# Optimization experiments

Measured on AMD Instinct MI355X. Metric: run time of the kernel, lower is better.

The kernel has to match this reference:

```python
import jax, jax.numpy as jnp
from jax import lax
import numpy as np

N_CENTER, N_NEAR, COUT = 1024, 32, 256


def fps(xyz, m):
    # farthest point sampling -> [B, m] int32 indices
    B, N, _ = xyz.shape
    dist0 = jnp.full((B, N), 1e10, xyz.dtype)
    far0 = jnp.zeros((B,), jnp.int32)

    def step(carry, _):
        dists, far = carry
        cen = jax.vmap(lambda p, i: p[i])(xyz, far)            # [B,3]
        d = jnp.sum((xyz - cen[:, None, :]) ** 2, axis=-1)     # [B,N]
        dists = jnp.minimum(dists, d)
        nxt = jnp.argmax(dists, axis=-1).astype(jnp.int32)
        return (dists, nxt), far

    _, idx = lax.scan(step, (dist0, far0), None, length=m)
    return jnp.transpose(idx)                                   # [B,m]


def knn(xyz, k):
    # euclidean kNN over all points -> [B,N,k] (stand-in for surface_knn)
    sq = jnp.sum(xyz ** 2, axis=-1)                             # [B,N]
    d = sq[:, :, None] + sq[:, None, :] - 2.0 * jnp.einsum('bnd,bmd->bnm', xyz, xyz)
    _, idx = lax.top_k(-d, k)
    return idx


def gather(x, idx):
    # index_points: x [B,N,...], idx [B,S] or [B,S,K]
    return jax.vmap(lambda p, i: p[i])(x, idx)


def point_attention(center_fea, group_fea, wq, wk, wv):
    # center_fea [B,S,Cin], group_fea [B,S,K,D] -> [B,S,COUT]
    q = jnp.einsum('bsc,ch->bsh', center_fea, wq)
    k = jnp.einsum('bskd,dh->bskh', group_fea, wk)
    v = jnp.einsum('bskd,dh->bskh', group_fea, wv)
    scores = jnp.einsum('bsh,bskh->bsk', q, k) / jnp.sqrt(jnp.asarray(COUT, q.dtype))
    attn = jax.nn.softmax(scores, axis=-1)
    return jnp.einsum('bsk,bskh->bsh', attn, v)


def _forward(xyz, mad, adj, pt, mad_fea, adj_fea, pt_fea, cst_fea,
             wq_mad, wk_mad, wv_mad, wq_adj, wk_adj, wv_adj,
             wq_pt, wk_pt, wv_pt, wq_cst, wk_cst, wv_cst):
    idx_all = knn(xyz, N_NEAR)                  # [B,N,K]
    fps_idx = fps(xyz, N_CENTER)                # [B,S]

    center_xyz = gather(xyz, fps_idx)
    center_mad = gather(mad, fps_idx)
    center_adj = gather(adj, fps_idx)
    center_pt = gather(pt, fps_idx)
    c_mad_fea = gather(mad_fea, fps_idx)
    c_adj_fea = gather(adj_fea, fps_idx)
    c_pt_fea = gather(pt_fea, fps_idx)
    c_cst_fea = gather(cst_fea, fps_idx)

    idx = gather(idx_all, fps_idx)              # [B,S,K]
    g_xyz = gather(xyz, idx)
    g_mad = gather(mad, idx)
    g_adj = gather(adj, idx)
    g_pt = gather(pt, idx)
    g_mad_fea = gather(mad_fea, idx)
    g_adj_fea = gather(adj_fea, idx)
    g_pt_fea = gather(pt_fea, idx)
    g_cst_fea = gather(cst_fea, idx)

    mad_rel = g_mad - center_mad[:, :, None, :]
    adj_cat = jnp.concatenate([g_adj, jnp.broadcast_to(center_adj[:, :, None, :], g_adj.shape)], axis=-1)
    pt_cat = jnp.concatenate([g_pt, jnp.broadcast_to(center_pt[:, :, None, :], g_pt.shape)], axis=-1)
    xyz_rel = g_xyz - center_xyz[:, :, None, :]

    g_mad_fea = jnp.concatenate([g_mad_fea, mad_rel], axis=-1)
    g_adj_fea = jnp.concatenate([g_adj_fea, adj_cat], axis=-1)
    g_pt_fea = jnp.concatenate([g_pt_fea, pt_cat], axis=-1)
    g_cst_fea = jnp.concatenate([g_cst_fea, xyz_rel], axis=-1)

    o_mad = point_attention(c_mad_fea, g_mad_fea, wq_mad, wk_mad, wv_mad)
    o_adj = point_attention(c_adj_fea, g_adj_fea, wq_adj, wk_adj, wv_adj)
    o_pt = point_attention(c_pt_fea, g_pt_fea, wq_pt, wk_pt, wv_pt)
    o_cst = point_attention(c_cst_fea, g_cst_fea, wq_cst, wk_cst, wv_cst)

    return (center_xyz, center_mad, center_adj, center_pt, o_mad, o_adj, o_pt, o_cst)


def setup_inputs() -> dict:
    key = jax.random.key(0)
    ks = jax.random.split(key, 24)
    B, N, C = 4, 4096, 128
    inp = {
        'xyz': jax.random.normal(ks[0], (B, N, 3), jnp.float32),
        'mad': jax.random.normal(ks[1], (B, N, 3), jnp.float32),
        'adj': jax.random.uniform(ks[2], (B, N, 2), jnp.float32),
        'pt': jax.random.uniform(ks[3], (B, N, 4), jnp.float32),
        'mad_fea': jax.random.normal(ks[4], (B, N, C), jnp.float32),
        'adj_fea': jax.random.normal(ks[5], (B, N, C), jnp.float32),
        'pt_fea': jax.random.normal(ks[6], (B, N, C), jnp.float32),
        'cst_fea': jax.random.normal(ks[7], (B, N, C), jnp.float32),
    }
    dims = {'wq_mad': C, 'wk_mad': C + 3, 'wv_mad': C + 3,
            'wq_adj': C, 'wk_adj': C + 4, 'wv_adj': C + 4,
            'wq_pt': C, 'wk_pt': C + 8, 'wv_pt': C + 8,
            'wq_cst': C, 'wk_cst': C + 3, 'wv_cst': C + 3}
    for i, (name, d) in enumerate(dims.items()):
        inp[name] = jax.random.normal(ks[8 + i], (d, COUT), jnp.float32) * 0.02
    return inp


def reference(xyz, mad, adj, pt, mad_fea, adj_fea, pt_fea, cst_fea,
              wq_mad, wk_mad, wv_mad, wq_adj, wk_adj, wv_adj,
              wq_pt, wk_pt, wv_pt, wq_cst, wk_cst, wv_cst):
    return _forward(xyz, mad, adj, pt, mad_fea, adj_fea, pt_fea, cst_fea,
                    wq_mad, wk_mad, wv_mad, wq_adj, wk_adj, wv_adj,
                    wq_pt, wk_pt, wv_pt, wq_cst, wk_cst, wv_cst)
```

## Files before the change

kernel.cpp:

```cpp
#include <hip/hip_runtime.h>

#define BATCH 4
#define NPTS  4096
#define NC    1024
#define KNN   32
#define CIN   128
#define CO    256
#define DP    136

#define OFF_CXYZ 0
#define OFF_CMAD (BATCH*NC*3)
#define OFF_CADJ (OFF_CMAD + BATCH*NC*3)
#define OFF_CPT  (OFF_CADJ + BATCH*NC*2)
#define OFF_OMAD (OFF_CPT  + BATCH*NC*4)
#define OFF_OADJ (OFF_OMAD + BATCH*NC*CO)
#define OFF_OPT  (OFF_OADJ + BATCH*NC*CO)
#define OFF_OCST (OFF_OPT  + BATCH*NC*CO)

typedef unsigned long long u64;

template<bool MAXI>
__device__ __forceinline__ u64 wave_red_u64(u64 k)
{
    const int oldv = MAXI ? 0 : -1;
#define DPP_STEP(C)                                                              \
    {                                                                            \
        unsigned plo = (unsigned)__builtin_amdgcn_update_dpp(oldv, (int)(unsigned)k,        C, 0xf, 0xf, false); \
        unsigned phi = (unsigned)__builtin_amdgcn_update_dpp(oldv, (int)(unsigned)(k>>32),  C, 0xf, 0xf, false); \
        u64 p = ((u64)phi << 32) | plo;                                          \
        if (MAXI ? (p > k) : (p < k)) k = p;                                     \
    }
    DPP_STEP(0x111) DPP_STEP(0x112) DPP_STEP(0x114)
    DPP_STEP(0x118) DPP_STEP(0x142) DPP_STEP(0x143)
#undef DPP_STEP
    return k;
}

__global__ __launch_bounds__(256) void fps_prep_kernel(
    const float* __restrict__ xyz, int* __restrict__ fps_idx,
    const float* __restrict__ wq_mad, const float* __restrict__ wk_mad, const float* __restrict__ wv_mad,
    const float* __restrict__ wq_adj, const float* __restrict__ wk_adj, const float* __restrict__ wv_adj,
    const float* __restrict__ wq_pt,  const float* __restrict__ wk_pt,  const float* __restrict__ wv_pt,
    const float* __restrict__ wq_cst, const float* __restrict__ wk_cst, const float* __restrict__ wv_cst,
    float* __restrict__ M, float* __restrict__ Wvp)
{
    __shared__ float4 s_xyz[NPTS];
    __shared__ u64    s_ck[2][4];
    const int t = threadIdx.x;

    if (blockIdx.x >= BATCH) {
        const int r    = blockIdx.x - BATCH;
        const int type = r / DP;
        const int row  = r - type * DP;
        const float* wq; const float* wk; const float* wv; int D;
        if (type == 0)      { wq=wq_mad; wk=wk_mad; wv=wv_mad; D=131; }
        else if (type == 1) { wq=wq_adj; wk=wk_adj; wv=wv_adj; D=132; }
        else if (type == 2) { wq=wq_pt;  wk=wk_pt;  wv=wv_pt;  D=136; }
        else                { wq=wq_cst; wk=wk_cst; wv=wv_cst; D=131; }

        Wvp[((size_t)type*DP + row)*CO + t] = (row < D) ? wv[(size_t)row*CO + t] : 0.f;

        if (row < CIN) {
            float* sq = (float*)s_xyz;
            sq[t] = wq[(size_t)row*CO + t];
            __syncthreads();
            if (t < DP) {
                float acc = 0.f;
                if (t < D) {
                    const float* wkr = wk + (size_t)t * CO;
                    for (int h = 0; h < CO; h += 4) {
                        float4 a = *(const float4*)&wkr[h];
                        float4 b4 = *(const float4*)&sq[h];
                        acc = fmaf(a.x,b4.x,acc); acc = fmaf(a.y,b4.y,acc);
                        acc = fmaf(a.z,b4.z,acc); acc = fmaf(a.w,b4.w,acc);
                    }
                }
                M[((size_t)type*CIN + row)*DP + t] = acc;
            }
        }
        return;
    }

    const int b = blockIdx.x;
    const float* xb = xyz + (size_t)b * NPTS * 3;

    float px[16], py[16], pz[16], dd[16];
    unsigned pv[16];
#pragma unroll
    for (int i = 0; i < 16; ++i) {
        int p = t + i * 256;
        px[i] = xb[p*3+0]; py[i] = xb[p*3+1]; pz[i] = xb[p*3+2];
        s_xyz[p] = make_float4(px[i], py[i], pz[i], 0.f);
        dd[i] = 1e10f;
        pv[i] = (unsigned)p;
    }
    __syncthreads();

    int far = 0;
    float cx = xb[0], cy = xb[1], cz = xb[2];
    for (int s = 0; s < NC; ++s) {
        if (t == 0) fps_idx[b*NC + s] = far;

        float    gm[4] = {-1.f, -1.f, -1.f, -1.f};
        unsigned gi[4] = {0u, 0u, 0u, 0u};
#pragma unroll
        for (int i = 0; i < 16; ++i) {
            float dx = __fsub_rn(px[i], cx);
            float dy = __fsub_rn(py[i], cy);
            float dz = __fsub_rn(pz[i], cz);
            float d  = __fadd_rn(__fadd_rn(__fmul_rn(dx,dx), __fmul_rn(dy,dy)), __fmul_rn(dz,dz));
            float nd = fminf(dd[i], d);
            dd[i] = nd;
            const int g = i >> 2;
            if (nd > gm[g]) gi[g] = pv[i];
            gm[g] = fmaxf(gm[g], nd);
        }
        bool c1 = gm[1] > gm[0]; float a0 = c1 ? gm[1] : gm[0]; unsigned b0 = c1 ? gi[1] : gi[0];
        bool c3 = gm[3] > gm[2]; float a1 = c3 ? gm[3] : gm[2]; unsigned b1 = c3 ? gi[3] : gi[2];
        bool cf = a1 > a0;       float am = cf ? a1 : a0;       unsigned bm = cf ? b1 : b0;
        u64 k = ((u64)__float_as_uint(am) << 32) | (u64)(unsigned)~bm;

        k = wave_red_u64<true>(k);

        const int buf = s & 1;
        if ((t & 63) == 63) s_ck[buf][t>>6] = k;
        __syncthreads();
        u64 k0 = s_ck[buf][0], k1 = s_ck[buf][1], k2 = s_ck[buf][2], k3 = s_ck[buf][3];
        float4 c0 = s_xyz[(int)~((unsigned)k0)];
        float4 c1v = s_xyz[(int)~((unsigned)k1)];
        float4 c2v = s_xyz[(int)~((unsigned)k2)];
        float4 c3v = s_xyz[(int)~((unsigned)k3)];
        bool m1 = k1 > k0; u64 ka = m1 ? k1 : k0; float4 ca = m1 ? c1v : c0;
        bool m3 = k3 > k2; u64 kb = m3 ? k3 : k2; float4 cb = m3 ? c3v : c2v;
        bool mf = kb > ka; u64 kw = mf ? kb : ka; float4 cw = mf ? cb : ca;
        far = (int)~((unsigned)kw);
        cx = cw.x; cy = cw.y; cz = cw.z;
    }
}

__global__ __launch_bounds__(256) void knn_kernel(const float* __restrict__ xyz,
                                                  const int* __restrict__ fps_idx,
                                                  int* __restrict__ nbr_idx)
{
    const int bs = blockIdx.x;
    const int b  = bs >> 10;
    const int t  = threadIdx.x;
    const float* xb = xyz + (size_t)b * NPTS * 3;
    const int ci = fps_idx[bs];
    const float cx = xb[ci*3], cy = xb[ci*3+1], cz = xb[ci*3+2];
    const float sqc = __fadd_rn(__fadd_rn(__fmul_rn(cx,cx), __fmul_rn(cy,cy)), __fmul_rn(cz,cz));

    u64 key[16];
#pragma unroll
    for (int i = 0; i < 16; ++i) {
        int p = t + i * 256;
        float x = xb[p*3], y = xb[p*3+1], z = xb[p*3+2];
        float sqm = __fadd_rn(__fadd_rn(__fmul_rn(x,x), __fmul_rn(y,y)), __fmul_rn(z,z));
        float dot = __fadd_rn(__fadd_rn(__fmul_rn(cx,x), __fmul_rn(cy,y)), __fmul_rn(cz,z));
        float dv  = __fsub_rn(__fadd_rn(sqc, sqm), __fmul_rn(2.0f, dot));
        unsigned u = __float_as_uint(dv);
        u ^= (unsigned)(((int)u >> 31)) | 0x80000000u;
        key[i] = ((u64)u << 32) | (unsigned)p;
    }
    u64 kmin = key[0];
#pragma unroll
    for (int i = 1; i < 16; ++i) if (key[i] < kmin) kmin = key[i];

    __shared__ u64 s_ck[2][4];

    for (int kk = 0; kk < KNN; ++kk) {
        u64 k = wave_red_u64<false>(kmin);
        const int buf = kk & 1;
        if ((t & 63) == 63) s_ck[buf][t>>6] = k;
        __syncthreads();
        u64 k0 = s_ck[buf][0], k1 = s_ck[buf][1], k2 = s_ck[buf][2], k3 = s_ck[buf][3];
        if (k1 < k0) k0 = k1;
        if (k3 < k2) k2 = k3;
        if (k2 < k0) k0 = k2;
        unsigned w = (unsigned)k0;
        if (t == 0) nbr_idx[bs*KNN + kk] = (int)w;
        if ((w & 255u) == (unsigned)t) {
#pragma unroll
            for (int i = 0; i < 16; ++i)
                if (w == (unsigned)(t + i*256)) key[i] = ~0ull;
            u64 m = key[0];
#pragma unroll
            for (int i = 1; i < 16; ++i) if (key[i] < m) m = key[i];
            kmin = m;
        }
    }
}

template<int TYPE>
__device__ __forceinline__ void attn_t(
    int b, int bs0, int ci,
    const float* __restrict__ fea, const float* __restrict__ aux,
    const float* __restrict__ Mt, const float* __restrict__ Wvpt,
    float* __restrict__ outp,
    float (*s_cf)[CIN], float (*s_u)[DP], float (*s_fea)[KNN][DP],
    float (*s_sc)[KNN], float (*s_wf)[DP], const int (*s_nbr4)[KNN])
{
    const int t = threadIdx.x, g = t >> 6, l = t & 63;
    const int l31 = l & 31, h32 = l >> 5;

    if (l < 32) {
        float4 v = *(const float4*)&fea[((size_t)(b*NPTS + ci))*CIN + l*4];
        *(float4*)&s_cf[g][l*4] = v;
    }
#pragma unroll
    for (int it = 0; it < 16; ++it) {
        int kk = it*2 + h32;
        int j  = s_nbr4[g][kk];
        float4 v = *(const float4*)&fea[((size_t)(b*NPTS + j))*CIN + l31*4];
        *(float4*)&s_fea[g][kk][l31*4] = v;
    }
    if (l < KNN) {
        int j = s_nbr4[g][l];
        float pad[8];
        if (TYPE == 0 || TYPE == 3) {
#pragma unroll
            for (int i = 0; i < 3; ++i)
                pad[i] = aux[(size_t)(b*NPTS + j)*3 + i] - aux[(size_t)(b*NPTS + ci)*3 + i];
            pad[3]=pad[4]=pad[5]=pad[6]=pad[7]=0.f;
        } else if (TYPE == 1) {
            pad[0] = aux[(size_t)(b*NPTS + j)*2 + 0];
            pad[1] = aux[(size_t)(b*NPTS + j)*2 + 1];
            pad[2] = aux[(size_t)(b*NPTS + ci)*2 + 0];
            pad[3] = aux[(size_t)(b*NPTS + ci)*2 + 1];
            pad[4]=pad[5]=pad[6]=pad[7]=0.f;
        } else {
#pragma unroll
            for (int i = 0; i < 4; ++i) pad[i]   = aux[(size_t)(b*NPTS + j)*4 + i];
#pragma unroll
            for (int i = 0; i < 4; ++i) pad[4+i] = aux[(size_t)(b*NPTS + ci)*4 + i];
        }
#pragma unroll
        for (int i = 0; i < 8; ++i) s_fea[g][l][CIN+i] = pad[i];
    }
    __syncthreads();

#pragma unroll
    for (int j = 0; j < 3; ++j) {
        int d = l + 64*j;
        if (d < DP) {
            float acc = 0.f;
            for (int c = 0; c < CIN; c += 4) {
                float4 cf4 = *(const float4*)&s_cf[g][c];
                acc = fmaf(cf4.x, Mt[(size_t)(c+0)*DP + d], acc);
                acc = fmaf(cf4.y, Mt[(size_t)(c+1)*DP + d], acc);
                acc = fmaf(cf4.z, Mt[(size_t)(c+2)*DP + d], acc);
                acc = fmaf(cf4.w, Mt[(size_t)(c+3)*DP + d], acc);
            }
            s_u[g][d] = acc;
        }
    }
    __syncthreads();

#pragma unroll
    for (int it = 0; it < 16; ++it) {
        int kk = it*2 + h32;
        float acc = 0.f;
        for (int c = l31; c < DP/4; c += 32) {
            float4 f4 = *(const float4*)&s_fea[g][kk][c*4];
            float4 u4 = *(const float4*)&s_u[g][c*4];
            acc = fmaf(f4.x,u4.x,acc); acc = fmaf(f4.y,u4.y,acc);
            acc = fmaf(f4.z,u4.z,acc); acc = fmaf(f4.w,u4.w,acc);
        }
#pragma unroll
        for (int off = 16; off; off >>= 1) acc += __shfl_xor(acc, off);
        if (l31 == 0) s_sc[g][kk] = acc * 0.0625f;
    }
    __syncthreads();

    if (l < KNN) {
        float sc = s_sc[g][l];
        float m = sc;
#pragma unroll
        for (int off = 16; off; off >>= 1) m = fmaxf(m, __shfl_xor(m, off));
        float e = expf(sc - m);
        float ssum = e;
#pragma unroll
        for (int off = 16; off; off >>= 1) ssum += __shfl_xor(ssum, off);
        s_sc[g][l] = e / ssum;
    }
    __syncthreads();

    if (l < DP/4) {
        const int d0 = l*4;
        float w0=0.f, w1=0.f, w2=0.f, w3=0.f;
#pragma unroll
        for (int k4 = 0; k4 < KNN; k4 += 4) {
            float4 a  = *(const float4*)&s_sc[g][k4];
            float4 f0 = *(const float4*)&s_fea[g][k4+0][d0];
            float4 f1 = *(const float4*)&s_fea[g][k4+1][d0];
            float4 f2 = *(const float4*)&s_fea[g][k4+2][d0];
            float4 f3 = *(const float4*)&s_fea[g][k4+3][d0];
            w0=fmaf(a.x,f0.x,w0); w1=fmaf(a.x,f0.y,w1); w2=fmaf(a.x,f0.z,w2); w3=fmaf(a.x,f0.w,w3);
            w0=fmaf(a.y,f1.x,w0); w1=fmaf(a.y,f1.y,w1); w2=fmaf(a.y,f1.z,w2); w3=fmaf(a.y,f1.w,w3);
            w0=fmaf(a.z,f2.x,w0); w1=fmaf(a.z,f2.y,w1); w2=fmaf(a.z,f2.z,w2); w3=fmaf(a.z,f2.w,w3);
            w0=fmaf(a.w,f3.x,w0); w1=fmaf(a.w,f3.y,w1); w2=fmaf(a.w,f3.z,w2); w3=fmaf(a.w,f3.w,w3);
        }
        s_wf[g][d0+0]=w0; s_wf[g][d0+1]=w1; s_wf[g][d0+2]=w2; s_wf[g][d0+3]=w3;
    }
    __syncthreads();

    float o0=0.f, o1=0.f, o2=0.f, o3=0.f;
    for (int d4 = 0; d4 < DP/4; ++d4) {
        float4 wf0 = *(const float4*)&s_wf[0][d4*4];
        float4 wf1 = *(const float4*)&s_wf[1][d4*4];
        float4 wf2 = *(const float4*)&s_wf[2][d4*4];
        float4 wf3 = *(const float4*)&s_wf[3][d4*4];
        float v0 = Wvpt[(size_t)(d4*4+0)*CO + t];
        float v1 = Wvpt[(size_t)(d4*4+1)*CO + t];
        float v2 = Wvpt[(size_t)(d4*4+2)*CO + t];
        float v3 = Wvpt[(size_t)(d4*4+3)*CO + t];
        o0=fmaf(wf0.x,v0,o0); o0=fmaf(wf0.y,v1,o0); o0=fmaf(wf0.z,v2,o0); o0=fmaf(wf0.w,v3,o0);
        o1=fmaf(wf1.x,v0,o1); o1=fmaf(wf1.y,v1,o1); o1=fmaf(wf1.z,v2,o1); o1=fmaf(wf1.w,v3,o1);
        o2=fmaf(wf2.x,v0,o2); o2=fmaf(wf2.y,v1,o2); o2=fmaf(wf2.z,v2,o2); o2=fmaf(wf2.w,v3,o2);
        o3=fmaf(wf3.x,v0,o3); o3=fmaf(wf3.y,v1,o3); o3=fmaf(wf3.z,v2,o3); o3=fmaf(wf3.w,v3,o3);
    }
    outp[(size_t)(bs0+0)*CO + t] = o0;
    outp[(size_t)(bs0+1)*CO + t] = o1;
    outp[(size_t)(bs0+2)*CO + t] = o2;
    outp[(size_t)(bs0+3)*CO + t] = o3;
    __syncthreads();
}

__global__ __launch_bounds__(256) void attn_kernel(
    const float* __restrict__ xyz, const float* __restrict__ mad,
    const float* __restrict__ adj, const float* __restrict__ pt,
    const float* __restrict__ mad_fea, const float* __restrict__ adj_fea,
    const float* __restrict__ pt_fea,  const float* __restrict__ cst_fea,
    const float* __restrict__ M, const float* __restrict__ Wvp,
    const int* __restrict__ fps_idx, const int* __restrict__ nbr_idx,
    float* __restrict__ out)
{
    __shared__ float s_cf[4][CIN];
    __shared__ float s_u[4][DP];
    __shared__ float s_fea[4][KNN][DP];
    __shared__ float s_sc[4][KNN];
    __shared__ float s_wf[4][DP];
    __shared__ int   s_nbr4[4][KNN];
    __shared__ int   s_ci4[4];

    const int bs0 = blockIdx.x * 4;
    const int b   = bs0 >> 10;
    const int t   = threadIdx.x;
    const int g   = t >> 6, l = t & 63;

    if (t < 4) s_ci4[t] = fps_idx[bs0 + t];
    if (t < 128) s_nbr4[t>>5][t&31] = nbr_idx[(bs0 + (t>>5))*KNN + (t&31)];
    __syncthreads();
    const int ci = s_ci4[g];

    if (l < 3)             out[OFF_CXYZ + (bs0+g)*3 + l]      = xyz[(size_t)(b*NPTS+ci)*3 + l];
    if (l >= 4 && l < 7)   out[OFF_CMAD + (bs0+g)*3 + (l-4)]  = mad[(size_t)(b*NPTS+ci)*3 + (l-4)];
    if (l >= 8 && l < 10)  out[OFF_CADJ + (bs0+g)*2 + (l-8)]  = adj[(size_t)(b*NPTS+ci)*2 + (l-8)];
    if (l >= 12 && l < 16) out[OFF_CPT  + (bs0+g)*4 + (l-12)] = pt[(size_t)(b*NPTS+ci)*4 + (l-12)];

    attn_t<0>(b, bs0, ci, mad_fea, mad, M + 0*CIN*DP, Wvp + 0*DP*CO, out + OFF_OMAD,
              s_cf, s_u, s_fea, s_sc, s_wf, s_nbr4);
    attn_t<1>(b, bs0, ci, adj_fea, adj, M + 1*CIN*DP, Wvp + 1*DP*CO, out + OFF_OADJ,
              s_cf, s_u, s_fea, s_sc, s_wf, s_nbr4);
    attn_t<2>(b, bs0, ci, pt_fea,  pt,  M + 2*CIN*DP, Wvp + 2*DP*CO, out + OFF_OPT,
              s_cf, s_u, s_fea, s_sc, s_wf, s_nbr4);
    attn_t<3>(b, bs0, ci, cst_fea, xyz, M + 3*CIN*DP, Wvp + 3*DP*CO, out + OFF_OCST,
              s_cf, s_u, s_fea, s_sc, s_wf, s_nbr4);
}

extern "C" void kernel_launch(void* const* d_in, const int* in_sizes, int n_in,
                              void* d_out, int out_size, void* d_ws, size_t ws_size,
                              hipStream_t stream)
{
    const float* xyz     = (const float*)d_in[0];
    const float* mad     = (const float*)d_in[1];
    const float* adj     = (const float*)d_in[2];
    const float* pt      = (const float*)d_in[3];
    const float* mad_fea = (const float*)d_in[4];
    const float* adj_fea = (const float*)d_in[5];
    const float* pt_fea  = (const float*)d_in[6];
    const float* cst_fea = (const float*)d_in[7];
    const float* wq_mad  = (const float*)d_in[8];
    const float* wk_mad  = (const float*)d_in[9];
    const float* wv_mad  = (const float*)d_in[10];
    const float* wq_adj  = (const float*)d_in[11];
    const float* wk_adj  = (const float*)d_in[12];
    const float* wv_adj  = (const float*)d_in[13];
    const float* wq_pt   = (const float*)d_in[14];
    const float* wk_pt   = (const float*)d_in[15];
    const float* wv_pt   = (const float*)d_in[16];
    const float* wq_cst  = (const float*)d_in[17];
    const float* wk_cst  = (const float*)d_in[18];
    const float* wv_cst  = (const float*)d_in[19];
    float* out = (float*)d_out;

    int*   fps_idx = (int*)d_ws;
    int*   nbr_idx = fps_idx + BATCH*NC;
    float* M       = (float*)(nbr_idx + BATCH*NC*KNN);
    float* Wvp     = M + 4*CIN*DP;

    fps_prep_kernel<<<BATCH + 4*DP, 256, 0, stream>>>(xyz, fps_idx,
        wq_mad, wk_mad, wv_mad, wq_adj, wk_adj, wv_adj,
        wq_pt, wk_pt, wv_pt, wq_cst, wk_cst, wv_cst, M, Wvp);
    knn_kernel<<<BATCH*NC, 256, 0, stream>>>(xyz, fps_idx, nbr_idx);
    attn_kernel<<<BATCH*NC/4, 256, 0, stream>>>(xyz, mad, adj, pt,
        mad_fea, adj_fea, pt_fea, cst_fea, M, Wvp, fps_idx, nbr_idx, out);
}
```

Measured before the change: 1.121 ms.

## Interleave two batches' farthest point sampling per block to share barriers

```diff
diff --git a/kernel.cpp b/kernel.cpp
--- a/kernel.cpp
+++ b/kernel.cpp
@@ -36,6 +36,29 @@
     return k;
 }
 
+__device__ __forceinline__ u64 fps_step(const float* px, const float* py, const float* pz,
+                                        float* dd, float cx, float cy, float cz, int t)
+{
+    float    gm[4] = {-1.f, -1.f, -1.f, -1.f};
+    unsigned gi[4] = {0u, 0u, 0u, 0u};
+#pragma unroll
+    for (int i = 0; i < 16; ++i) {
+        float dx = __fsub_rn(px[i], cx);
+        float dy = __fsub_rn(py[i], cy);
+        float dz = __fsub_rn(pz[i], cz);
+        float d  = __fadd_rn(__fadd_rn(__fmul_rn(dx,dx), __fmul_rn(dy,dy)), __fmul_rn(dz,dz));
+        float nd = fminf(dd[i], d);
+        dd[i] = nd;
+        const int g = i >> 2;
+        if (nd > gm[g]) gi[g] = (unsigned)(t + i*256);
+        gm[g] = fmaxf(gm[g], nd);
+    }
+    bool c1 = gm[1] > gm[0]; float a0 = c1 ? gm[1] : gm[0]; unsigned b0 = c1 ? gi[1] : gi[0];
+    bool c3 = gm[3] > gm[2]; float a1 = c3 ? gm[3] : gm[2]; unsigned b1 = c3 ? gi[3] : gi[2];
+    bool cf = a1 > a0;       float am = cf ? a1 : a0;       unsigned bm = cf ? b1 : b0;
+    return ((u64)__float_as_uint(am) << 32) | (u64)(unsigned)~bm;
+}
+
 __global__ __launch_bounds__(256) void fps_prep_kernel(
     const float* __restrict__ xyz, int* __restrict__ fps_idx,
     const float* __restrict__ wq_mad, const float* __restrict__ wk_mad, const float* __restrict__ wv_mad,
@@ -44,12 +67,13 @@
     const float* __restrict__ wq_cst, const float* __restrict__ wk_cst, const float* __restrict__ wv_cst,
     float* __restrict__ M, float* __restrict__ Wvp)
 {
-    __shared__ float4 s_xyz[NPTS];
-    __shared__ u64    s_ck[2][4];
+    __shared__ float2 s_xy[2][NPTS];
+    __shared__ float  s_z [2][NPTS];
+    __shared__ u64    s_ck[2][2][4];
     const int t = threadIdx.x;
 
-    if (blockIdx.x >= BATCH) {
-        const int r    = blockIdx.x - BATCH;
+    if (blockIdx.x >= 2) {
+        const int r    = blockIdx.x - 2;
         const int type = r / DP;
         const int row  = r - type * DP;
         const float* wq; const float* wk; const float* wv; int D;
@@ -61,7 +85,7 @@
         Wvp[((size_t)type*DP + row)*CO + t] = (row < D) ? wv[(size_t)row*CO + t] : 0.f;
 
         if (row < CIN) {
-            float* sq = (float*)s_xyz;
+            float* sq = (float*)s_xy;
             sq[t] = wq[(size_t)row*CO + t];
             __syncthreads();
             if (t < DP) {
@@ -81,60 +105,58 @@
         return;
     }
 
-    const int b = blockIdx.x;
-    const float* xb = xyz + (size_t)b * NPTS * 3;
-
-    float px[16], py[16], pz[16], dd[16];
-    unsigned pv[16];
+    const int b0 = blockIdx.x * 2, b1 = b0 + 1;
+    const float* xb0 = xyz + (size_t)b0 * NPTS * 3;
+    const float* xb1 = xyz + (size_t)b1 * NPTS * 3;
+
+    float px0[16], py0[16], pz0[16], dd0[16];
+    float px1[16], py1[16], pz1[16], dd1[16];
 #pragma unroll
     for (int i = 0; i < 16; ++i) {
         int p = t + i * 256;
-        px[i] = xb[p*3+0]; py[i] = xb[p*3+1]; pz[i] = xb[p*3+2];
-        s_xyz[p] = make_float4(px[i], py[i], pz[i], 0.f);
-        dd[i] = 1e10f;
-        pv[i] = (unsigned)p;
-    }
-    __syncthreads();
-
-    int far = 0;
-    float cx = xb[0], cy = xb[1], cz = xb[2];
+        px0[i] = xb0[p*3+0]; py0[i] = xb0[p*3+1]; pz0[i] = xb0[p*3+2];
+        px1[i] = xb1[p*3+0]; py1[i] = xb1[p*3+1]; pz1[i] = xb1[p*3+2];
+        s_xy[0][p] = make_float2(px0[i], py0[i]); s_z[0][p] = pz0[i];
+        s_xy[1][p] = make_float2(px1[i], py1[i]); s_z[1][p] = pz1[i];
+        dd0[i] = 1e10f; dd1[i] = 1e10f;
+    }
+    __syncthreads();
+
+    int farA = 0, farB = 0;
+    float cxA = xb0[0], cyA = xb0[1], czA = xb0[2];
+    float cxB = xb1[0], cyB = xb1[1], czB = xb1[2];
+
     for (int s = 0; s < NC; ++s) {
-        if (t == 0) fps_idx[b*NC + s] = far;
-
-        float    gm[4] = {-1.f, -1.f, -1.f, -1.f};
-        unsigned gi[4] = {0u, 0u, 0u, 0u};
-#pragma unroll
-        for (int i = 0; i < 16; ++i) {
-            float dx = __fsub_rn(px[i], cx);
-            float dy = __fsub_rn(py[i], cy);
-            float dz = __fsub_rn(pz[i], cz);
-            float d  = __fadd_rn(__fadd_rn(__fmul_rn(dx,dx), __fmul_rn(dy,dy)), __fmul_rn(dz,dz));
-            float nd = fminf(dd[i], d);
-            dd[i] = nd;
-            const int g = i >> 2;
-            if (nd > gm[g]) gi[g] = pv[i];
-            gm[g] = fmaxf(gm[g], nd);
-        }
-        bool c1 = gm[1] > gm[0]; float a0 = c1 ? gm[1] : gm[0]; unsigned b0 = c1 ? gi[1] : gi[0];
-        bool c3 = gm[3] > gm[2]; float a1 = c3 ? gm[3] : gm[2]; unsigned b1 = c3 ? gi[3] : gi[2];
-        bool cf = a1 > a0;       float am = cf ? a1 : a0;       unsigned bm = cf ? b1 : b0;
-        u64 k = ((u64)__float_as_uint(am) << 32) | (u64)(unsigned)~bm;
-
-        k = wave_red_u64<true>(k);
-
+        if (t == 0) {
+            fps_idx[b0*NC + s] = farA;
+            fps_idx[b1*NC + s] = farB;
+        }
         const int buf = s & 1;
-        if ((t & 63) == 63) s_ck[buf][t>>6] = k;
+
+        u64 kA = fps_step(px0, py0, pz0, dd0, cxA, cyA, czA, t);
+        kA = wave_red_u64<true>(kA);
+        if ((t & 63) == 63) s_ck[0][buf][t>>6] = kA;
+
+        u64 kB = fps_step(px1, py1, pz1, dd1, cxB, cyB, czB, t);
+        kB = wave_red_u64<true>(kB);
+        if ((t & 63) == 63) s_ck[1][buf][t>>6] = kB;
+
         __syncthreads();
-        u64 k0 = s_ck[buf][0], k1 = s_ck[buf][1], k2 = s_ck[buf][2], k3 = s_ck[buf][3];
-        float4 c0 = s_xyz[(int)~((unsigned)k0)];
-        float4 c1v = s_xyz[(int)~((unsigned)k1)];
-        float4 c2v = s_xyz[(int)~((unsigned)k2)];
-        float4 c3v = s_xyz[(int)~((unsigned)k3)];
-        bool m1 = k1 > k0; u64 ka = m1 ? k1 : k0; float4 ca = m1 ? c1v : c0;
-        bool m3 = k3 > k2; u64 kb = m3 ? k3 : k2; float4 cb = m3 ? c3v : c2v;
-        bool mf = kb > ka; u64 kw = mf ? kb : ka; float4 cw = mf ? cb : ca;
-        far = (int)~((unsigned)kw);
-        cx = cw.x; cy = cw.y; cz = cw.z;
+
+        u64 a0 = s_ck[0][buf][0], a1 = s_ck[0][buf][1], a2 = s_ck[0][buf][2], a3 = s_ck[0][buf][3];
+        u64 e0 = s_ck[1][buf][0], e1 = s_ck[1][buf][1], e2 = s_ck[1][buf][2], e3 = s_ck[1][buf][3];
+        if (a1 > a0) a0 = a1;
+        if (a3 > a2) a2 = a3;
+        if (a2 > a0) a0 = a2;
+        if (e1 > e0) e0 = e1;
+        if (e3 > e2) e2 = e3;
+        if (e2 > e0) e0 = e2;
+        farA = (int)~((unsigned)a0);
+        farB = (int)~((unsigned)e0);
+        float2 ca = s_xy[0][farA]; float za = s_z[0][farA];
+        float2 cb = s_xy[1][farB]; float zb = s_z[1][farB];
+        cxA = ca.x; cyA = ca.y; czA = za;
+        cxB = cb.x; cyB = cb.y; czB = zb;
     }
 }
 
@@ -399,7 +421,7 @@
     float* M       = (float*)(nbr_idx + BATCH*NC*KNN);
     float* Wvp     = M + 4*CIN*DP;
 
-    fps_prep_kernel<<<BATCH + 4*DP, 256, 0, stream>>>(xyz, fps_idx,
+    fps_prep_kernel<<<2 + 4*DP, 256, 0, stream>>>(xyz, fps_idx,
         wq_mad, wk_mad, wv_mad, wq_adj, wk_adj, wv_adj,
         wq_pt, wk_pt, wv_pt, wq_cst, wk_cst, wv_cst, M, Wvp);
     knn_kernel<<<BATCH*NC, 256, 0, stream>>>(xyz, fps_idx, nbr_idx);
```

Result: slower. 1.638 ms (+46.1%).
